# Optimization experiments

Hardware: AMD Instinct MI355X
Metric: run time of the kernel (lower is better)

## Reference

```python
import jax, jax.numpy as jnp
from jax import lax
import numpy as np

NUM_POINT = 1024
RADIUS = 0.4
NSAMPLE = 32


def setup_inputs() -> dict:
    key = jax.random.key(0)
    ks = jax.random.split(key, 16)
    B, N, C = 8, 16384, 64
    chans = [67, 64, 128, 256]
    inp = {
        "points_xyz": jax.random.normal(ks[0], (B, N, 3), jnp.float32),
        "features": jax.random.normal(ks[1], (B, C, N), jnp.float32),
    }
    ki = 2
    for l, (cin, cout) in enumerate(zip(chans[:-1], chans[1:])):
        inp[f"W{l}"] = jax.random.normal(ks[ki], (cout, cin), jnp.float32) * (1.0 / np.sqrt(cin)); ki += 1
        inp[f"b{l}"] = jax.random.normal(ks[ki], (cout,), jnp.float32) * 0.02; ki += 1
        inp[f"s{l}"] = jax.random.uniform(ks[ki], (cout,), jnp.float32, 0.5, 1.5); ki += 1
        inp[f"t{l}"] = jax.random.normal(ks[ki], (cout,), jnp.float32) * 0.02; ki += 1
    return inp


def farthest_point_sample(xyz, npoint):
    # xyz: (B, N, 3) -> idx (B, npoint) int32. D-FPS starting at index 0.
    B, N, _ = xyz.shape

    def step(carry, _):
        dists, farthest = carry  # (B,N), (B,)
        centroid = jnp.take_along_axis(xyz, farthest[:, None, None], axis=1)  # (B,1,3)
        d = jnp.sum((xyz - centroid) ** 2, axis=-1)  # (B,N)
        dists = jnp.minimum(dists, d)
        nxt = jnp.argmax(dists, axis=-1).astype(jnp.int32)
        return (dists, nxt), farthest

    init = (jnp.full((B, N), 1e10, xyz.dtype), jnp.zeros((B,), jnp.int32))
    _, idx = lax.scan(step, init, None, length=npoint)
    return idx.T  # (B, npoint)


def ball_query(points_xyz, new_xyz, radius, nsample):
    # First-nsample-in-index-order points within radius; pad with first found
    # (semantics of the CUDA ball_query kernel in PointNet++/mmdet3d).
    B, N, _ = points_xyz.shape
    d2 = jnp.sum((new_xyz[:, :, None, :] - points_xyz[:, None, :, :]) ** 2, axis=-1)  # (B,M,N)
    arange = jnp.arange(N, dtype=jnp.float32)
    key = jnp.where(d2 <= radius * radius, arange, jnp.float32(N))
    neg_k, _ = lax.top_k(-key, nsample)  # smallest nsample keys
    idx = (-neg_k).astype(jnp.int32)  # (B,M,K)
    first = idx[..., :1]
    idx = jnp.where(idx < N, idx, first)  # pad empty slots with first neighbor
    return jnp.clip(idx, 0, N - 1)


def query_and_group(points_xyz, new_xyz, features, idx, use_xyz=True):
    # points_xyz (B,N,3), new_xyz (B,M,3), features (B,C,N), idx (B,M,K)
    B, N, _ = points_xyz.shape
    M, K = idx.shape[1], idx.shape[2]
    flat = idx.reshape(B, M * K)
    gxyz = jnp.take_along_axis(points_xyz, flat[:, :, None], axis=1).reshape(B, M, K, 3)
    gxyz = gxyz - new_xyz[:, :, None, :]  # relative coords
    gxyz = jnp.transpose(gxyz, (0, 3, 1, 2))  # (B,3,M,K)
    gfeat = jnp.take_along_axis(features, flat[:, None, :], axis=2).reshape(B, -1, M, K)
    if use_xyz:
        return jnp.concatenate([gxyz, gfeat], axis=1)  # (B, 3+C, M, K)
    return gfeat


def mlp_layer(x, W, b, s, t):
    # 1x1 Conv2d + folded BatchNorm (per-channel scale/shift) + ReLU
    y = jnp.einsum("oc,bcmk->bomk", W, x) + b[None, :, None, None]
    y = y * s[None, :, None, None] + t[None, :, None, None]
    return jax.nn.relu(y)


def reference(points_xyz, features, W0, b0, s0, t0, W1, b1, s1, t1, W2, b2, s2, t2):
    indices = farthest_point_sample(points_xyz, NUM_POINT)  # (B,M)
    new_xyz = jnp.take_along_axis(points_xyz, indices[:, :, None], axis=1)  # (B,M,3)
    idx = ball_query(points_xyz, new_xyz, RADIUS, NSAMPLE)  # (B,M,K)
    g = query_and_group(points_xyz, new_xyz, features, idx, use_xyz=True)  # (B,67,M,K)
    h = mlp_layer(g, W0, b0, s0, t0)
    h = mlp_layer(h, W1, b1, s1, t1)
    h = mlp_layer(h, W2, b2, s2, t2)  # (B,256,M,K)
    new_features = jnp.max(h, axis=-1)  # max pool over K -> (B,256,M)
    return new_xyz, new_features, indices
```

## Files before the change

### kernel.cpp

```cpp
#include <hip/hip_runtime.h>
#include <stdint.h>

#define NB 8
#define NPT 16384
#define NM 1024
#define NK 32

#define WS_W0T 0
#define WS_B0  (WS_W0T + 4288)
#define WS_W1T (WS_B0 + 64)
#define WS_B1  (WS_W1T + 8192)
#define WS_W2T (WS_B1 + 128)
#define WS_B2  (WS_W2T + 32768)
#define WS_IDX (WS_B2 + 256)
#define WS_NXYZ (WS_IDX + 8192)
#define WS_BALL (WS_NXYZ + 24576)

#define OUT_XYZ 0
#define OUT_FEAT 24576
#define OUT_IDX (24576 + 2097152)

__global__ void prep_weights(const float* __restrict__ W0, const float* __restrict__ b0,
                             const float* __restrict__ s0, const float* __restrict__ t0,
                             const float* __restrict__ W1, const float* __restrict__ b1,
                             const float* __restrict__ s1, const float* __restrict__ t1,
                             const float* __restrict__ W2, const float* __restrict__ b2,
                             const float* __restrict__ s2, const float* __restrict__ t2,
                             float* __restrict__ ws) {
    int id = blockIdx.x * 256 + threadIdx.x;
    if (id < 4288) { int c = id >> 6, o = id & 63;  ws[WS_W0T + id] = W0[o * 67 + c] * s0[o]; return; }
    id -= 4288;
    if (id < 64)   { ws[WS_B0 + id] = fmaf(b0[id], s0[id], t0[id]); return; }
    id -= 64;
    if (id < 8192) { int c = id >> 7, o = id & 127; ws[WS_W1T + id] = W1[o * 64 + c] * s1[o]; return; }
    id -= 8192;
    if (id < 128)  { ws[WS_B1 + id] = fmaf(b1[id], s1[id], t1[id]); return; }
    id -= 128;
    if (id < 32768){ int c = id >> 8, o = id & 255; ws[WS_W2T + id] = W2[o * 128 + c] * s2[o]; return; }
    id -= 32768;
    if (id < 256)  { ws[WS_B2 + id] = fmaf(b2[id], s2[id], t2[id]); return; }
}

#define FOREACH16(M) M(0) M(1) M(2) M(3) M(4) M(5) M(6) M(7) \
                     M(8) M(9) M(10) M(11) M(12) M(13) M(14) M(15)

template <int CTRL>
__device__ __forceinline__ uint32_t dpp_max_step(uint32_t v) {
    uint32_t o = (uint32_t)__builtin_amdgcn_update_dpp((int)v, (int)v, CTRL, 0xf, 0xf, false);
    return v > o ? v : o;
}
__device__ __forceinline__ uint32_t wave_max_u32(uint32_t v) {
    v = dpp_max_step<0x111>(v);
    v = dpp_max_step<0x112>(v);
    v = dpp_max_step<0x114>(v);
    v = dpp_max_step<0x118>(v);
    v = dpp_max_step<0x142>(v);
    v = dpp_max_step<0x143>(v);
    return v;
}
__device__ __forceinline__ uint32_t row_max_u32(uint32_t v) {
    v = dpp_max_step<0x111>(v);
    v = dpp_max_step<0x112>(v);
    v = dpp_max_step<0x114>(v);
    v = dpp_max_step<0x118>(v);
    return v;
}

__global__ __attribute__((amdgpu_flat_work_group_size(1024, 1024)))
void fps7_kernel(const float* __restrict__ xyz, int* __restrict__ out_idx) {
    __shared__ float2 pxy[NPT];
    __shared__ uint2 s_red[2][16];
    int b = blockIdx.x, t = threadIdx.x;
    const float* __restrict__ Xp = xyz + (size_t)b * NPT * 3;

#define DECL_PT(j) float pz##j, dd##j;
    FOREACH16(DECL_PT)
#undef DECL_PT

#define LOAD_PT(j) { int p = t + (j) * 1024; \
        float x = Xp[p * 3 + 0], y = Xp[p * 3 + 1]; \
        pz##j = Xp[p * 3 + 2]; \
        pxy[p] = make_float2(x, y); \
        dd##j = 1e10f; }
    FOREACH16(LOAD_PT)
#undef LOAD_PT
    __syncthreads();

    int farthest = 0;
    float cx = Xp[0], cy = Xp[1], cz = Xp[2];
    int lane = t & 63, w = t >> 6;
    for (int it = 0; it < NM; ++it) {
        if (t == 0) out_idx[b * NM + it] = farthest;
        float best = -1.0f; int bi = 0;
#define STEP_PT(j) { \
        float2 q = pxy[t + (j) * 1024]; \
        float dx = __fsub_rn(q.x, cx); \
        float dy = __fsub_rn(q.y, cy); \
        float dz = __fsub_rn(pz##j, cz); \
        float d  = __fadd_rn(__fadd_rn(__fmul_rn(dx, dx), __fmul_rn(dy, dy)), __fmul_rn(dz, dz)); \
        dd##j = fminf(dd##j, d); \
        if (dd##j > best) { best = dd##j; bi = t + (j) * 1024; } }
        FOREACH16(STEP_PT)
#undef STEP_PT
        uint32_t bbits = __float_as_uint(best);
        uint32_t wmax = __builtin_amdgcn_readlane(wave_max_u32(bbits), 63);
        uint32_t cand = (bbits == wmax) ? ~(uint32_t)bi : 0u;
        uint32_t cwin = __builtin_amdgcn_readlane(wave_max_u32(cand), 63);
        if (lane == 0) s_red[it & 1][w] = make_uint2(cwin, wmax);
        __syncthreads();
        uint2 e = s_red[it & 1][lane & 15];
        uint32_t hmax = __builtin_amdgcn_readlane(row_max_u32(e.y), 15);
        uint32_t c2 = (e.y == hmax) ? e.x : 0u;
        uint32_t c2w = __builtin_amdgcn_readlane(row_max_u32(c2), 15);
        int widx = (int)(~c2w);
        farthest = widx;
        const float* cp = Xp + (size_t)widx * 3;
        cx = cp[0]; cy = cp[1]; cz = cp[2];
    }
}

__global__ void gather_newxyz(const float* __restrict__ xyz, const int* __restrict__ idx_ws,
                              float* __restrict__ nxyz_ws, float* __restrict__ out_xyz,
                              float* __restrict__ out_idx_f) {
    int id = blockIdx.x * 256 + threadIdx.x;
    if (id >= NB * NM) return;
    int b = id / NM;
    int p = idx_ws[id];
    const float* Xp = xyz + ((size_t)b * NPT + p) * 3;
    float x = Xp[0], y = Xp[1], z = Xp[2];
    nxyz_ws[id * 3 + 0] = x; nxyz_ws[id * 3 + 1] = y; nxyz_ws[id * 3 + 2] = z;
    out_xyz[id * 3 + 0] = x; out_xyz[id * 3 + 1] = y; out_xyz[id * 3 + 2] = z;
    out_idx_f[id] = (float)p;
}

__global__ __launch_bounds__(256) void ball_query_kernel(const float* __restrict__ xyz,
                                                         const float* __restrict__ nxyz,
                                                         int* __restrict__ ball) {
    int blk = blockIdx.x;
    int b = blk >> 10;
    int t = threadIdx.x;
    const float* Xp = xyz + (size_t)b * NPT * 3;
    float cx = nxyz[blk * 3 + 0], cy = nxyz[blk * 3 + 1], cz = nxyz[blk * 3 + 2];
    const float r2 = (float)(0.4 * 0.4);
    uint64_t mask = 0;
    int base = t * 64;
    const float4* q = (const float4*)(Xp + (size_t)base * 3);
#pragma unroll 4
    for (int c = 0; c < 16; c++) {
        float4 A = q[c * 3 + 0], B = q[c * 3 + 1], C = q[c * 3 + 2];
        float xs[4] = {A.x, A.w, B.z, C.y};
        float ys[4] = {A.y, B.x, B.w, C.z};
        float zs[4] = {A.z, B.y, C.x, C.w};
#pragma unroll
        for (int u = 0; u < 4; u++) {
            float dx = __fsub_rn(xs[u], cx);
            float dy = __fsub_rn(ys[u], cy);
            float dz = __fsub_rn(zs[u], cz);
            float d2 = __fadd_rn(__fadd_rn(__fmul_rn(dx, dx), __fmul_rn(dy, dy)), __fmul_rn(dz, dz));
            if (d2 <= r2) mask |= (1ull << (c * 4 + u));
        }
    }
    int cnt = __popcll(mask);
    int scan = cnt;
    for (int off = 1; off < 64; off <<= 1) {
        int nv = __shfl_up(scan, off);
        if ((t & 63) >= off) scan += nv;
    }
    __shared__ int s_wsum[4];
    __shared__ int s_hit[32];
    int w = t >> 6;
    if ((t & 63) == 63) s_wsum[w] = scan;
    __syncthreads();
    int woff = 0;
    for (int i = 0; i < 4; i++) if (i < w) woff += s_wsum[i];
    int excl = woff + scan - cnt;
    uint64_t mm = mask; int pos = excl;
    while (mm && pos < 32) {
        int j = __ffsll((long long)mm) - 1;
        s_hit[pos] = base + j;
        pos++;
        mm &= mm - 1;
    }
    __syncthreads();
    int total = s_wsum[0] + s_wsum[1] + s_wsum[2] + s_wsum[3];
    if (t < 32) {
        int first = s_hit[0];
        ball[blk * NK + t] = (t < total) ? s_hit[t] : first;
    }
}

__global__ __attribute__((amdgpu_flat_work_group_size(256, 256), amdgpu_waves_per_eu(2, 2)))
void fused_mlp_kernel(const float* __restrict__ xyz,
                      const float* __restrict__ feats,
                      const float* __restrict__ ws_f,
                      const int* __restrict__ ball,
                      const float* __restrict__ nxyz,
                      float* __restrict__ out_feat) {
    int blk = blockIdx.x;
    int b = blk >> 9;
    int m0 = (blk & 511) * 2;
    int t = threadIdx.x;
    int k = t & 31, g = t >> 5;
    __shared__ float Xs[2][67][32];
    __shared__ float h1[2][64][32];
    __shared__ float h2[2][128][32];
    __shared__ int sidx[2][32];
    const float* W0t = ws_f + WS_W0T; const float* b0f = ws_f + WS_B0;
    const float* W1t = ws_f + WS_W1T; const float* b1f = ws_f + WS_B1;
    const float* W2t = ws_f + WS_W2T; const float* b2f = ws_f + WS_B2;

    if (t < 64) {
        int ctr = t >> 5;
        sidx[ctr][t & 31] = ball[((size_t)b * NM + m0 + ctr) * NK + (t & 31)];
    }
    __syncthreads();

    const float* Xp = xyz + (size_t)b * NPT * 3;
    if (g < 6) {
        int ctr = g / 3, dim = g % 3;
        float cc = nxyz[((size_t)b * NM + m0 + ctr) * 3 + dim];
        Xs[ctr][dim][k] = Xp[sidx[ctr][k] * 3 + dim] - cc;
    }
    const float* Fp = feats + (size_t)b * 64 * NPT;
#pragma unroll
    for (int i = 0; i < 8; i++) {
        int c = g + 8 * i;
        Xs[0][3 + c][k] = Fp[(size_t)c * NPT + sidx[0][k]];
        Xs[1][3 + c][k] = Fp[(size_t)c * NPT + sidx[1][k]];
    }
    __syncthreads();

    {
        float acc0[8], acc1[8];
#pragma unroll
        for (int i = 0; i < 8; i++) { acc0[i] = b0f[g * 8 + i]; acc1[i] = acc0[i]; }
#pragma unroll 4
        for (int c = 0; c < 67; c++) {
            float xv0 = Xs[0][c][k], xv1 = Xs[1][c][k];
            const float* wr = W0t + c * 64 + g * 8;
            float4 wa = *(const float4*)(wr), wb = *(const float4*)(wr + 4);
            acc0[0] = fmaf(wa.x, xv0, acc0[0]); acc1[0] = fmaf(wa.x, xv1, acc1[0]);
            acc0[1] = fmaf(wa.y, xv0, acc0[1]); acc1[1] = fmaf(wa.y, xv1, acc1[1]);
            acc0[2] = fmaf(wa.z, xv0, acc0[2]); acc1[2] = fmaf(wa.z, xv1, acc1[2]);
            acc0[3] = fmaf(wa.w, xv0, acc0[3]); acc1[3] = fmaf(wa.w, xv1, acc1[3]);
            acc0[4] = fmaf(wb.x, xv0, acc0[4]); acc1[4] = fmaf(wb.x, xv1, acc1[4]);
            acc0[5] = fmaf(wb.y, xv0, acc0[5]); acc1[5] = fmaf(wb.y, xv1, acc1[5]);
            acc0[6] = fmaf(wb.z, xv0, acc0[6]); acc1[6] = fmaf(wb.z, xv1, acc1[6]);
            acc0[7] = fmaf(wb.w, xv0, acc0[7]); acc1[7] = fmaf(wb.w, xv1, acc1[7]);
        }
#pragma unroll
        for (int i = 0; i < 8; i++) {
            h1[0][g * 8 + i][k] = fmaxf(acc0[i], 0.0f);
            h1[1][g * 8 + i][k] = fmaxf(acc1[i], 0.0f);
        }
    }
    __syncthreads();

    {
        float acc0[16], acc1[16];
#pragma unroll
        for (int i = 0; i < 16; i++) { acc0[i] = b1f[g * 16 + i]; acc1[i] = acc0[i]; }
#pragma unroll 4
        for (int c = 0; c < 64; c++) {
            float xv0 = h1[0][c][k], xv1 = h1[1][c][k];
            const float4* wr = (const float4*)(W1t + c * 128 + g * 16);
#pragma unroll
            for (int q = 0; q < 4; q++) {
                float4 wv = wr[q];
                acc0[q * 4 + 0] = fmaf(wv.x, xv0, acc0[q * 4 + 0]); acc1[q * 4 + 0] = fmaf(wv.x, xv1, acc1[q * 4 + 0]);
                acc0[q * 4 + 1] = fmaf(wv.y, xv0, acc0[q * 4 + 1]); acc1[q * 4 + 1] = fmaf(wv.y, xv1, acc1[q * 4 + 1]);
                acc0[q * 4 + 2] = fmaf(wv.z, xv0, acc0[q * 4 + 2]); acc1[q * 4 + 2] = fmaf(wv.z, xv1, acc1[q * 4 + 2]);
                acc0[q * 4 + 3] = fmaf(wv.w, xv0, acc0[q * 4 + 3]); acc1[q * 4 + 3] = fmaf(wv.w, xv1, acc1[q * 4 + 3]);
            }
        }
#pragma unroll
        for (int i = 0; i < 16; i++) {
            h2[0][g * 16 + i][k] = fmaxf(acc0[i], 0.0f);
            h2[1][g * 16 + i][k] = fmaxf(acc1[i], 0.0f);
        }
    }
    __syncthreads();

#pragma unroll
    for (int half = 0; half < 2; half++) {
        float acc0[16], acc1[16];
#pragma unroll
        for (int i = 0; i < 16; i++) { acc0[i] = b2f[g * 32 + half * 16 + i]; acc1[i] = acc0[i]; }
#pragma unroll 4
        for (int c = 0; c < 128; c++) {
            float xv0 = h2[0][c][k], xv1 = h2[1][c][k];
            const float4* wr = (const float4*)(W2t + c * 256 + g * 32 + half * 16);
#pragma unroll
            for (int q = 0; q < 4; q++) {
                float4 wv = wr[q];
                acc0[q * 4 + 0] = fmaf(wv.x, xv0, acc0[q * 4 + 0]); acc1[q * 4 + 0] = fmaf(wv.x, xv1, acc1[q * 4 + 0]);
                acc0[q * 4 + 1] = fmaf(wv.y, xv0, acc0[q * 4 + 1]); acc1[q * 4 + 1] = fmaf(wv.y, xv1, acc1[q * 4 + 1]);
                acc0[q * 4 + 2] = fmaf(wv.z, xv0, acc0[q * 4 + 2]); acc1[q * 4 + 2] = fmaf(wv.z, xv1, acc1[q * 4 + 2]);
                acc0[q * 4 + 3] = fmaf(wv.w, xv0, acc0[q * 4 + 3]); acc1[q * 4 + 3] = fmaf(wv.w, xv1, acc1[q * 4 + 3]);
            }
        }
#pragma unroll
        for (int i = 0; i < 16; i++) {
            float v0 = fmaxf(acc0[i], 0.0f);
            float v1 = fmaxf(acc1[i], 0.0f);
#pragma unroll
            for (int off = 16; off >= 1; off >>= 1) {
                v0 = fmaxf(v0, __shfl_xor(v0, off));
                v1 = fmaxf(v1, __shfl_xor(v1, off));
            }
            if (k == 0) {
                size_t o = (size_t)b * 256 + g * 32 + half * 16 + i;
                out_feat[o * NM + m0]     = v0;
                out_feat[o * NM + m0 + 1] = v1;
            }
        }
    }
}

extern "C" void kernel_launch(void* const* d_in, const int* in_sizes, int n_in,
                              void* d_out, int out_size, void* d_ws, size_t ws_size,
                              hipStream_t stream) {
    const float* xyz   = (const float*)d_in[0];
    const float* feats = (const float*)d_in[1];
    const float* W0 = (const float*)d_in[2];  const float* b0 = (const float*)d_in[3];
    const float* s0 = (const float*)d_in[4];  const float* t0 = (const float*)d_in[5];
    const float* W1 = (const float*)d_in[6];  const float* b1 = (const float*)d_in[7];
    const float* s1 = (const float*)d_in[8];  const float* t1 = (const float*)d_in[9];
    const float* W2 = (const float*)d_in[10]; const float* b2 = (const float*)d_in[11];
    const float* s2 = (const float*)d_in[12]; const float* t2 = (const float*)d_in[13];

    float* ws_f = (float*)d_ws;
    int*   idx_ws  = (int*)(ws_f + WS_IDX);
    float* nxyz_ws = ws_f + WS_NXYZ;
    int*   ball_ws = (int*)(ws_f + WS_BALL);

    float* out_f = (float*)d_out;
    float* out_xyz  = out_f + OUT_XYZ;
    float* out_feat = out_f + OUT_FEAT;
    float* out_idxf = out_f + OUT_IDX;

    prep_weights<<<179, 256, 0, stream>>>(W0, b0, s0, t0, W1, b1, s1, t1, W2, b2, s2, t2, ws_f);
    fps7_kernel<<<NB, 1024, 0, stream>>>(xyz, idx_ws);
    gather_newxyz<<<32, 256, 0, stream>>>(xyz, idx_ws, nxyz_ws, out_xyz, out_idxf);
    ball_query_kernel<<<NB * NM, 256, 0, stream>>>(xyz, nxyz_ws, ball_ws);
    fused_mlp_kernel<<<NB * NM / 2, 256, 0, stream>>>(xyz, feats, ws_f, ball_ws, nxyz_ws, out_feat);
}
```

Measured before the change: 2.720 ms.

## Use packed f32 math in FPS and alias MLP smem for higher occupancy

The FPS kernel now stores point x/y pairs as swizzled float4s in shared memory and computes squared distances for two points at once using v_pk_add_f32/v_pk_mul_f32 inline asm. This halves the VALU instruction count and LDS loads in the serial 1024-step loop, which dominates runtime with only 8 blocks. The fused MLP kernel reuses one shared buffer for the input and layer-2 activations, adding a barrier, so shared memory shrinks and waves_per_eu can rise from 2 to 3. Packed math is exact per lane, so FPS tie-breaking should match, but higher occupancy may limit registers and cause spills.

```diff
diff --git a/kernel.cpp b/kernel.cpp
--- a/kernel.cpp
+++ b/kernel.cpp
@@ -19,6 +19,8 @@
 #define OUT_XYZ 0
 #define OUT_FEAT 24576
 #define OUT_IDX (24576 + 2097152)
+
+typedef float fx2 __attribute__((ext_vector_type(2)));
 
 __global__ void prep_weights(const float* __restrict__ W0, const float* __restrict__ b0,
                              const float* __restrict__ s0, const float* __restrict__ t0,
@@ -41,8 +43,7 @@
     if (id < 256)  { ws[WS_B2 + id] = fmaf(b2[id], s2[id], t2[id]); return; }
 }
 
-#define FOREACH16(M) M(0) M(1) M(2) M(3) M(4) M(5) M(6) M(7) \
-                     M(8) M(9) M(10) M(11) M(12) M(13) M(14) M(15)
+#define FOREACH8(M) M(0) M(1) M(2) M(3) M(4) M(5) M(6) M(7)
 
 template <int CTRL>
 __device__ __forceinline__ uint32_t dpp_max_step(uint32_t v) {
@@ -67,23 +68,24 @@
 }
 
 __global__ __attribute__((amdgpu_flat_work_group_size(1024, 1024)))
-void fps7_kernel(const float* __restrict__ xyz, int* __restrict__ out_idx) {
-    __shared__ float2 pxy[NPT];
+void fps8_kernel(const float* __restrict__ xyz, int* __restrict__ out_idx) {
+    __shared__ float4 P4[NPT / 2];
     __shared__ uint2 s_red[2][16];
     int b = blockIdx.x, t = threadIdx.x;
     const float* __restrict__ Xp = xyz + (size_t)b * NPT * 3;
-
-#define DECL_PT(j) float pz##j, dd##j;
-    FOREACH16(DECL_PT)
-#undef DECL_PT
-
-#define LOAD_PT(j) { int p = t + (j) * 1024; \
-        float x = Xp[p * 3 + 0], y = Xp[p * 3 + 1]; \
-        pz##j = Xp[p * 3 + 2]; \
-        pxy[p] = make_float2(x, y); \
-        dd##j = 1e10f; }
-    FOREACH16(LOAD_PT)
-#undef LOAD_PT
+    int t7 = t & 7;
+
+#define DECL_PAIR(p) fx2 zz##p; float ddA##p, ddB##p;
+    FOREACH8(DECL_PAIR)
+#undef DECL_PAIR
+
+#define LOAD_PAIR(p) { int j0 = t + (2 * (p)) * 1024, j1 = t + (2 * (p) + 1) * 1024; \
+        float x0 = Xp[j0 * 3 + 0], y0 = Xp[j0 * 3 + 1]; zz##p.x = Xp[j0 * 3 + 2]; \
+        float x1 = Xp[j1 * 3 + 0], y1 = Xp[j1 * 3 + 1]; zz##p.y = Xp[j1 * 3 + 2]; \
+        P4[(t << 3) | ((p) ^ t7)] = make_float4(x0, x1, y0, y1); \
+        ddA##p = 1e10f; ddB##p = 1e10f; }
+    FOREACH8(LOAD_PAIR)
+#undef LOAD_PAIR
     __syncthreads();
 
     int farthest = 0;
@@ -91,17 +93,29 @@
     int lane = t & 63, w = t >> 6;
     for (int it = 0; it < NM; ++it) {
         if (t == 0) out_idx[b * NM + it] = farthest;
+        float mcx = -cx, mcy = -cy, mcz = -cz;
+        fx2 ncx; ncx.x = mcx; ncx.y = mcx;
+        fx2 ncy; ncy.x = mcy; ncy.y = mcy;
+        fx2 ncz; ncz.x = mcz; ncz.y = mcz;
         float best = -1.0f; int bi = 0;
-#define STEP_PT(j) { \
-        float2 q = pxy[t + (j) * 1024]; \
-        float dx = __fsub_rn(q.x, cx); \
-        float dy = __fsub_rn(q.y, cy); \
-        float dz = __fsub_rn(pz##j, cz); \
-        float d  = __fadd_rn(__fadd_rn(__fmul_rn(dx, dx), __fmul_rn(dy, dy)), __fmul_rn(dz, dz)); \
-        dd##j = fminf(dd##j, d); \
-        if (dd##j > best) { best = dd##j; bi = t + (j) * 1024; } }
-        FOREACH16(STEP_PT)
-#undef STEP_PT
+#define STEP_PAIR(p) { float4 A = P4[(t << 3) | ((p) ^ t7)]; \
+        fx2 xx; xx.x = A.x; xx.y = A.y; \
+        fx2 yy; yy.x = A.z; yy.y = A.w; \
+        fx2 dx, dy, dz, sxy, d; \
+        asm("v_pk_add_f32 %0, %1, %2" : "=v"(dx) : "v"(xx), "v"(ncx)); \
+        asm("v_pk_add_f32 %0, %1, %2" : "=v"(dy) : "v"(yy), "v"(ncy)); \
+        asm("v_pk_add_f32 %0, %1, %2" : "=v"(dz) : "v"(zz##p), "v"(ncz)); \
+        asm("v_pk_mul_f32 %0, %1, %1" : "=v"(dx) : "v"(dx)); \
+        asm("v_pk_mul_f32 %0, %1, %1" : "=v"(dy) : "v"(dy)); \
+        asm("v_pk_mul_f32 %0, %1, %1" : "=v"(dz) : "v"(dz)); \
+        asm("v_pk_add_f32 %0, %1, %2" : "=v"(sxy) : "v"(dx), "v"(dy)); \
+        asm("v_pk_add_f32 %0, %1, %2" : "=v"(d) : "v"(sxy), "v"(dz)); \
+        ddA##p = fminf(ddA##p, d.x); \
+        if (ddA##p > best) { best = ddA##p; bi = t + (2 * (p)) * 1024; } \
+        ddB##p = fminf(ddB##p, d.y); \
+        if (ddB##p > best) { best = ddB##p; bi = t + (2 * (p) + 1) * 1024; } }
+        FOREACH8(STEP_PAIR)
+#undef STEP_PAIR
         uint32_t bbits = __float_as_uint(best);
         uint32_t wmax = __builtin_amdgcn_readlane(wave_max_u32(bbits), 63);
         uint32_t cand = (bbits == wmax) ? ~(uint32_t)bi : 0u;
@@ -189,7 +203,7 @@
     }
 }
 
-__global__ __attribute__((amdgpu_flat_work_group_size(256, 256), amdgpu_waves_per_eu(2, 2)))
+__global__ __attribute__((amdgpu_flat_work_group_size(256, 256), amdgpu_waves_per_eu(3, 3)))
 void fused_mlp_kernel(const float* __restrict__ xyz,
                       const float* __restrict__ feats,
                       const float* __restrict__ ws_f,
@@ -201,9 +215,8 @@
     int m0 = (blk & 511) * 2;
     int t = threadIdx.x;
     int k = t & 31, g = t >> 5;
-    __shared__ float Xs[2][67][32];
+    __shared__ float u[2][128][32];
     __shared__ float h1[2][64][32];
-    __shared__ float h2[2][128][32];
     __shared__ int sidx[2][32];
     const float* W0t = ws_f + WS_W0T; const float* b0f = ws_f + WS_B0;
     const float* W1t = ws_f + WS_W1T; const float* b1f = ws_f + WS_B1;
@@ -219,14 +232,14 @@
     if (g < 6) {
         int ctr = g / 3, dim = g % 3;
         float cc = nxyz[((size_t)b * NM + m0 + ctr) * 3 + dim];
-        Xs[ctr][dim][k] = Xp[sidx[ctr][k] * 3 + dim] - cc;
+        u[ctr][dim][k] = Xp[sidx[ctr][k] * 3 + dim] - cc;
     }
     const float* Fp = feats + (size_t)b * 64 * NPT;
 #pragma unroll
     for (int i = 0; i < 8; i++) {
         int c = g + 8 * i;
-        Xs[0][3 + c][k] = Fp[(size_t)c * NPT + sidx[0][k]];
-        Xs[1][3 + c][k] = Fp[(size_t)c * NPT + sidx[1][k]];
+        u[0][3 + c][k] = Fp[(size_t)c * NPT + sidx[0][k]];
+        u[1][3 + c][k] = Fp[(size_t)c * NPT + sidx[1][k]];
     }
     __syncthreads();
 
@@ -236,7 +249,7 @@
         for (int i = 0; i < 8; i++) { acc0[i] = b0f[g * 8 + i]; acc1[i] = acc0[i]; }
 #pragma unroll 4
         for (int c = 0; c < 67; c++) {
-            float xv0 = Xs[0][c][k], xv1 = Xs[1][c][k];
+            float xv0 = u[0][c][k], xv1 = u[1][c][k];
             const float* wr = W0t + c * 64 + g * 8;
             float4 wa = *(const float4*)(wr), wb = *(const float4*)(wr + 4);
             acc0[0] = fmaf(wa.x, xv0, acc0[0]); acc1[0] = fmaf(wa.x, xv1, acc1[0]);
@@ -273,10 +286,11 @@
                 acc0[q * 4 + 3] = fmaf(wv.w, xv0, acc0[q * 4 + 3]); acc1[q * 4 + 3] = fmaf(wv.w, xv1, acc1[q * 4 + 3]);
             }
         }
+        __syncthreads();
 #pragma unroll
         for (int i = 0; i < 16; i++) {
-            h2[0][g * 16 + i][k] = fmaxf(acc0[i], 0.0f);
-            h2[1][g * 16 + i][k] = fmaxf(acc1[i], 0.0f);
+            u[0][g * 16 + i][k] = fmaxf(acc0[i], 0.0f);
+            u[1][g * 16 + i][k] = fmaxf(acc1[i], 0.0f);
         }
     }
     __syncthreads();
@@ -288,7 +302,7 @@
         for (int i = 0; i < 16; i++) { acc0[i] = b2f[g * 32 + half * 16 + i]; acc1[i] = acc0[i]; }
 #pragma unroll 4
         for (int c = 0; c < 128; c++) {
-            float xv0 = h2[0][c][k], xv1 = h2[1][c][k];
+            float xv0 = u[0][c][k], xv1 = u[1][c][k];
             const float4* wr = (const float4*)(W2t + c * 256 + g * 32 + half * 16);
 #pragma unroll
             for (int q = 0; q < 4; q++) {
@@ -340,7 +354,7 @@
     float* out_idxf = out_f + OUT_IDX;
 
     prep_weights<<<179, 256, 0, stream>>>(W0, b0, s0, t0, W1, b1, s1, t1, W2, b2, s2, t2, ws_f);
-    fps7_kernel<<<NB, 1024, 0, stream>>>(xyz, idx_ws);
+    fps8_kernel<<<NB, 1024, 0, stream>>>(xyz, idx_ws);
     gather_newxyz<<<32, 256, 0, stream>>>(xyz, idx_ws, nxyz_ws, out_xyz, out_idxf);
     ball_query_kernel<<<NB * NM, 256, 0, stream>>>(xyz, nxyz_ws, ball_ws);
     fused_mlp_kernel<<<NB * NM / 2, 256, 0, stream>>>(xyz, feats, ws_f, ball_ws, nxyz_ws, out_feat);
```

Measured after the change: 2.771 ms. About the same (+1.9%).
